# Optimization experiments

Hardware: AMD Instinct MI355X
Metric: run time of the kernel (lower is better)

## Reference

```python
import jax, jax.numpy as jnp
import numpy as np


def setup_inputs() -> dict:
    key = jax.random.key(0)
    B, C, H, W = 256, 64, 64, 64
    x = jax.random.normal(key, (B, C, H, W), dtype=jnp.float32)
    return {
        "x": x,
        "m": jnp.zeros((C, H, W), dtype=jnp.float32),
        "s": jnp.zeros((C, H, W), dtype=jnp.float32),
        "neuron_nonzero": jnp.zeros((C, H, W), dtype=jnp.int32),
        "n_samples": jnp.zeros((1,), dtype=jnp.int32),
    }


def reference(x, m, s, neuron_nonzero, n_samples):
    """Welford running mean/variance update over the batch dim of x.

    Faithful to TorchWelfordEstimator.forward: sequential per-sample
    recurrence on (m, s, neuron_nonzero, n_samples). x is detached in the
    original, so we stop gradients through it. Returns the passthrough x
    plus the updated state, matching the buffer updates.
    """
    xd = jax.lax.stop_gradient(x)  # x.detach()

    def step(carry, xi):
        m, s, nn, n = carry  # m,s: (C,H,W); nn: (C,H,W) int; n: (1,) int
        nn = nn + (xi != 0.0).astype(jnp.int32)
        old_m = m
        m = m + (xi - m) / (n.astype(xi.dtype) + 1.0)  # n broadcasts (1,)->(C,H,W)
        s = s + (xi - m) * (xi - old_m)
        return (m, s, nn, n + 1), None

    (m, s, nn, n), _ = jax.lax.scan(step, (m, s, neuron_nonzero, n_samples), xd)
    return x, m, s, nn, n
```

## Files before the change

### kernel.cpp

```cpp
#include <hip/hip_runtime.h>


constexpr int kB = 256;
constexpr int kN = 64 * 64 * 64;
constexpr int kBlock = 256;

__global__ __launch_bounds__(kBlock) void welford_fused(
    const float* __restrict__ x,
    const float* __restrict__ m_in,
    const float* __restrict__ s_in,
    const int*   __restrict__ nn_in,
    const int*   __restrict__ n0_in,
    float* __restrict__ out)
{
    const int j4 = blockIdx.x * blockDim.x + threadIdx.x;
    const int j  = j4 * 4;
    if (j >= kN) return;

    float* out_x  = out;
    float* out_m  = out + (size_t)kB * kN;
    float* out_s  = out_m + kN;
    float* out_nn = out_s + kN;
    float* out_n  = out_nn + kN;

    float4 m = *(const float4*)(m_in + j);
    float4 s = *(const float4*)(s_in + j);
    int4  nni = *(const int4*)(nn_in + j);
    const int n0 = n0_in[0];

    float4 nn = make_float4((float)nni.x, (float)nni.y, (float)nni.z, (float)nni.w);

#pragma unroll 4
    for (int b = 0; b < kB; ++b) {
        const size_t off = (size_t)b * kN + j;
        const float4 v = *(const float4*)(x + off);
        *(float4*)(out_x + off) = v;

        const float inv = 1.0f / (float)(n0 + b + 1);

        {
            nn.x += (v.x != 0.0f) ? 1.0f : 0.0f;
            const float om = m.x;
            m.x = om + (v.x - om) * inv;
            s.x += (v.x - m.x) * (v.x - om);
        }
        {
            nn.y += (v.y != 0.0f) ? 1.0f : 0.0f;
            const float om = m.y;
            m.y = om + (v.y - om) * inv;
            s.y += (v.y - m.y) * (v.y - om);
        }
        {
            nn.z += (v.z != 0.0f) ? 1.0f : 0.0f;
            const float om = m.z;
            m.z = om + (v.z - om) * inv;
            s.z += (v.z - m.z) * (v.z - om);
        }
        {
            nn.w += (v.w != 0.0f) ? 1.0f : 0.0f;
            const float om = m.w;
            m.w = om + (v.w - om) * inv;
            s.w += (v.w - m.w) * (v.w - om);
        }
    }

    *(float4*)(out_m  + j) = m;
    *(float4*)(out_s  + j) = s;
    *(float4*)(out_nn + j) = nn;
    if (j4 == 0) out_n[0] = (float)(n0 + kB);
}

extern "C" void kernel_launch(void* const* d_in, const int* in_sizes, int n_in,
                              void* d_out, int out_size, void* d_ws, size_t ws_size,
                              hipStream_t stream) {
    const float* x     = (const float*)d_in[0];
    const float* m_in  = (const float*)d_in[1];
    const float* s_in  = (const float*)d_in[2];
    const int*   nn_in = (const int*)d_in[3];
    const int*   n0_in = (const int*)d_in[4];
    float* out = (float*)d_out;

    const int threads = kN / 4;
    dim3 grid(threads / kBlock), block(kBlock);
    welford_fused<<<grid, block, 0, stream>>>(x, m_in, s_in, nn_in, n0_in, out);
}
```

Baseline: 433.8 us.

## Use two elements per thread with double-buffered nontemporal batch prefetch

Each thread now handles two elements instead of four, which doubles the thread count to improve memory-level parallelism. The batch loop is software-pipelined with two register buffers of eight rows each, so the next group's loads are in flight while the current group is computed. Loads and stores of the streamed x and its passthrough copy use nontemporal builtins to avoid cache pollution. The cost is more register pressure and narrower 8-byte accesses.

Result: no change. 431.4 us (-0.5%).

```diff
diff --git a/kernel.cpp b/kernel.cpp
--- a/kernel.cpp
+++ b/kernel.cpp
@@ -4,6 +4,9 @@
 constexpr int kB = 256;
 constexpr int kN = 64 * 64 * 64;
 constexpr int kBlock = 256;
+constexpr int kG = 8;
+
+typedef float f32x2 __attribute__((ext_vector_type(2)));
 
 __global__ __launch_bounds__(kBlock) void welford_fused(
     const float* __restrict__ x,
@@ -13,8 +16,8 @@
     const int*   __restrict__ n0_in,
     float* __restrict__ out)
 {
-    const int j4 = blockIdx.x * blockDim.x + threadIdx.x;
-    const int j  = j4 * 4;
+    const int j2 = blockIdx.x * blockDim.x + threadIdx.x;
+    const int j  = j2 * 2;
     if (j >= kN) return;
 
     float* out_x  = out;
@@ -23,51 +26,75 @@
     float* out_nn = out_s + kN;
     float* out_n  = out_nn + kN;
 
-    float4 m = *(const float4*)(m_in + j);
-    float4 s = *(const float4*)(s_in + j);
-    int4  nni = *(const int4*)(nn_in + j);
+    f32x2 m = *(const f32x2*)(m_in + j);
+    f32x2 s = *(const f32x2*)(s_in + j);
+    const int2 nni = *(const int2*)(nn_in + j);
     const int n0 = n0_in[0];
 
-    float4 nn = make_float4((float)nni.x, (float)nni.y, (float)nni.z, (float)nni.w);
+    f32x2 nn;
+    nn.x = (float)nni.x;
+    nn.y = (float)nni.y;
 
-#pragma unroll 4
-    for (int b = 0; b < kB; ++b) {
-        const size_t off = (size_t)b * kN + j;
-        const float4 v = *(const float4*)(x + off);
-        *(float4*)(out_x + off) = v;
+    f32x2 va[kG], vb[kG];
 
-        const float inv = 1.0f / (float)(n0 + b + 1);
+#pragma unroll
+    for (int u = 0; u < kG; ++u)
+        va[u] = __builtin_nontemporal_load((const f32x2*)(x + (size_t)u * kN + j));
 
-        {
+    for (int b0 = 0; b0 < kB; b0 += 2 * kG) {
+#pragma unroll
+        for (int u = 0; u < kG; ++u)
+            vb[u] = __builtin_nontemporal_load(
+                (const f32x2*)(x + (size_t)(b0 + kG + u) * kN + j));
+
+#pragma unroll
+        for (int u = 0; u < kG; ++u) {
+            const int b = b0 + u;
+            const f32x2 v = va[u];
+            __builtin_nontemporal_store(v, (f32x2*)(out_x + (size_t)b * kN + j));
+            const float inv = 1.0f / (float)(n0 + b + 1);
+
             nn.x += (v.x != 0.0f) ? 1.0f : 0.0f;
-            const float om = m.x;
+            float om = m.x;
             m.x = om + (v.x - om) * inv;
             s.x += (v.x - m.x) * (v.x - om);
-        }
-        {
+
             nn.y += (v.y != 0.0f) ? 1.0f : 0.0f;
-            const float om = m.y;
+            om = m.y;
             m.y = om + (v.y - om) * inv;
             s.y += (v.y - m.y) * (v.y - om);
         }
-        {
-            nn.z += (v.z != 0.0f) ? 1.0f : 0.0f;
-            const float om = m.z;
-            m.z = om + (v.z - om) * inv;
-            s.z += (v.z - m.z) * (v.z - om);
+
+        if (b0 + 2 * kG < kB) {
+#pragma unroll
+            for (int u = 0; u < kG; ++u)
+                va[u] = __builtin_nontemporal_load(
+                    (const f32x2*)(x + (size_t)(b0 + 2 * kG + u) * kN + j));
         }
-        {
-            nn.w += (v.w != 0.0f) ? 1.0f : 0.0f;
-            const float om = m.w;
-            m.w = om + (v.w - om) * inv;
-            s.w += (v.w - m.w) * (v.w - om);
+
+#pragma unroll
+        for (int u = 0; u < kG; ++u) {
+            const int b = b0 + kG + u;
+            const f32x2 v = vb[u];
+            __builtin_nontemporal_store(v, (f32x2*)(out_x + (size_t)b * kN + j));
+            const float inv = 1.0f / (float)(n0 + b + 1);
+
+            nn.x += (v.x != 0.0f) ? 1.0f : 0.0f;
+            float om = m.x;
+            m.x = om + (v.x - om) * inv;
+            s.x += (v.x - m.x) * (v.x - om);
+
+            nn.y += (v.y != 0.0f) ? 1.0f : 0.0f;
+            om = m.y;
+            m.y = om + (v.y - om) * inv;
+            s.y += (v.y - m.y) * (v.y - om);
         }
     }
 
-    *(float4*)(out_m  + j) = m;
-    *(float4*)(out_s  + j) = s;
-    *(float4*)(out_nn + j) = nn;
-    if (j4 == 0) out_n[0] = (float)(n0 + kB);
+    *(f32x2*)(out_m  + j) = m;
+    *(f32x2*)(out_s  + j) = s;
+    *(f32x2*)(out_nn + j) = nn;
+    if (j2 == 0) out_n[0] = (float)(n0 + kB);
 }
 
 extern "C" void kernel_launch(void* const* d_in, const int* in_sizes, int n_in,
@@ -80,7 +107,7 @@
     const int*   n0_in = (const int*)d_in[4];
     float* out = (float*)d_out;
 
-    const int threads = kN / 4;
+    const int threads = kN / 2;
     dim3 grid(threads / kBlock), block(kBlock);
     welford_fused<<<grid, block, 0, stream>>>(x, m_in, s_in, nn_in, n0_in, out);
 }
```
